# Kernel tuning notes

Measured on AMD Instinct MI355X. Metric: run time of the kernel, lower is better.

Reference implementation:

```python
import jax, jax.numpy as jnp
import numpy as np
from jax import lax

TAU = 0.1
DT = 0.001
UNITS = 1024
B, T = 16, 2048


def setup_inputs() -> dict:
    key = jax.random.key(0)
    inputs = jax.random.normal(key, (B, T, UNITS), dtype=jnp.float32)
    level_var = jnp.zeros((1, UNITS), dtype=jnp.float32)
    e = np.exp(-DT / TAU)
    smoothing_init = np.log(e / (1.0 - e)).astype(np.float32)
    smoothing_var = jnp.ones((1, UNITS), dtype=jnp.float32) * smoothing_init
    return {"inputs": inputs, "level_var": level_var, "smoothing_var": smoothing_var}


def reference(inputs, level_var, smoothing_var):
    # inputs: [B, T, U]; level_var, smoothing_var: [1, U]
    s = jax.nn.sigmoid(smoothing_var)  # [1, U]
    level0 = jnp.broadcast_to(level_var, (inputs.shape[0], inputs.shape[2]))  # [B, U]

    def step(level, x_t):
        new = (1.0 - s) * x_t + s * level  # [B, U]
        return new, new

    _, levels = lax.scan(step, level0, jnp.swapaxes(inputs, 0, 1))  # [T, B, U]
    return jnp.swapaxes(levels, 0, 1)  # [B, T, U]
```

## Files before the change

### kernel.cpp

```cpp
#include <hip/hip_runtime.h>


constexpr int B = 16;
constexpr int T = 2048;
constexpr int U = 1024;
constexpr int D = 32;

__global__ __launch_bounds__(64, 1) void lowpass_kernel(
    const float* __restrict__ in,
    const float* __restrict__ level0,
    const float* __restrict__ smooth,
    float* __restrict__ out)
{
    const int lane = threadIdx.x;
    const int blk  = blockIdx.x;
    const int b    = blk >> 4;
    const int ublk = blk & 15;
    const int u    = (ublk << 6) + lane;

    const float sm  = smooth[u];
    const float s   = 1.0f / (1.0f + expf(-sm));
    const float oms = 1.0f - s;
    float level     = level0[u];

    const size_t base = (size_t)b * T * U + u;
    const float* __restrict__ ip = in  + base;
    float*       __restrict__ op = out + base;

    float buf[D];
    #pragma unroll
    for (int i = 0; i < D; ++i) buf[i] = ip[(size_t)i * U];

    int t = 0;
    for (; t < T - D; t += D) {
        #pragma unroll
        for (int j = 0; j < D; ++j) {
            float x = buf[j];
            buf[j] = ip[(size_t)(t + D + j) * U];
            level = fmaf(s, level, oms * x);
            op[(size_t)(t + j) * U] = level;
        }
    }
    #pragma unroll
    for (int j = 0; j < D; ++j) {
        float x = buf[j];
        level = fmaf(s, level, oms * x);
        op[(size_t)(t + j) * U] = level;
    }
}

extern "C" void kernel_launch(void* const* d_in, const int* in_sizes, int n_in,
                              void* d_out, int out_size, void* d_ws, size_t ws_size,
                              hipStream_t stream) {
    const float* in     = (const float*)d_in[0];
    const float* level0 = (const float*)d_in[1];
    const float* smooth = (const float*)d_in[2];
    float* out          = (float*)d_out;

    dim3 grid(B * (U / 64));
    dim3 block(64);
    hipLaunchKernelGGL(lowpass_kernel, grid, block, 0, stream,
                       in, level0, smooth, out);
}
```

Measured before the change: 253.7 us.

## Split time axis into chunks with two-pass chunked linear-recurrence scan

Splits the sequential recurrence over T into 8 chunks. A first kernel computes each chunk's zero-initialized end state into workspace. A second kernel combines the prior chunk states using s^L to get each chunk's starting level, then rescans the chunk and writes outputs. This raises the number of independent wavefronts eightfold to hide the serial dependency latency, at the cost of reading the input twice and an extra launch.

```diff
diff --git a/kernel.cpp b/kernel.cpp
--- a/kernel.cpp
+++ b/kernel.cpp
@@ -1,51 +1,107 @@
 #include <hip/hip_runtime.h>
 
 
-constexpr int B = 16;
-constexpr int T = 2048;
-constexpr int U = 1024;
-constexpr int D = 32;
+constexpr int B  = 16;
+constexpr int T  = 2048;
+constexpr int U  = 1024;
+constexpr int C  = 8;
+constexpr int L  = T / C;
+constexpr int D1 = 32;
+constexpr int D2 = 16;
+constexpr int BU = B * U;
 
-__global__ __launch_bounds__(64, 1) void lowpass_kernel(
+__device__ __forceinline__ float sigmoidf(float x) {
+    return 1.0f / (1.0f + __expf(-x));
+}
+
+__global__ __launch_bounds__(64, 2) void lowpass_partial(
+    const float* __restrict__ in,
+    const float* __restrict__ smooth,
+    float* __restrict__ P)
+{
+    const int lane = threadIdx.x;
+    const int blk  = blockIdx.x;
+    const int c    = blk >> 8;
+    const int r    = blk & 255;
+    const int b    = r >> 4;
+    const int u    = ((r & 15) << 6) + lane;
+
+    const float s   = sigmoidf(smooth[u]);
+    const float oms = 1.0f - s;
+
+    const float* __restrict__ ip = in + (size_t)b * T * U + (size_t)(c * L) * U + u;
+
+    float lv = 0.0f;
+    float buf[D1];
+    #pragma unroll
+    for (int i = 0; i < D1; ++i) buf[i] = ip[(size_t)i * U];
+
+    int t = 0;
+    for (; t < L - D1; t += D1) {
+        #pragma unroll
+        for (int j = 0; j < D1; ++j) {
+            float x = buf[j];
+            buf[j] = ip[(size_t)(t + D1 + j) * U];
+            lv = fmaf(s, lv, oms * x);
+        }
+    }
+    #pragma unroll
+    for (int j = 0; j < D1; ++j) {
+        lv = fmaf(s, lv, oms * buf[j]);
+    }
+
+    P[(size_t)c * BU + (size_t)b * U + u] = lv;
+}
+
+__global__ __launch_bounds__(64, 2) void lowpass_scan(
     const float* __restrict__ in,
     const float* __restrict__ level0,
     const float* __restrict__ smooth,
+    const float* __restrict__ P,
     float* __restrict__ out)
 {
     const int lane = threadIdx.x;
     const int blk  = blockIdx.x;
-    const int b    = blk >> 4;
-    const int ublk = blk & 15;
-    const int u    = (ublk << 6) + lane;
+    const int c    = blk >> 8;
+    const int r    = blk & 255;
+    const int b    = r >> 4;
+    const int u    = ((r & 15) << 6) + lane;
+    const int chain = b * U + u;
 
-    const float sm  = smooth[u];
-    const float s   = 1.0f / (1.0f + expf(-sm));
+    const float s   = sigmoidf(smooth[u]);
     const float oms = 1.0f - s;
-    float level     = level0[u];
 
-    const size_t base = (size_t)b * T * U + u;
+    float sL = s;
+    #pragma unroll
+    for (int i = 0; i < 8; ++i) sL *= sL;
+
+    float lv = level0[u];
+    for (int i = 0; i < c; ++i) {
+        lv = fmaf(sL, lv, P[(size_t)i * BU + chain]);
+    }
+
+    const size_t base = (size_t)b * T * U + (size_t)(c * L) * U + u;
     const float* __restrict__ ip = in  + base;
     float*       __restrict__ op = out + base;
 
-    float buf[D];
+    float buf[D2];
     #pragma unroll
-    for (int i = 0; i < D; ++i) buf[i] = ip[(size_t)i * U];
+    for (int i = 0; i < D2; ++i) buf[i] = ip[(size_t)i * U];
 
     int t = 0;
-    for (; t < T - D; t += D) {
+    for (; t < L - D2; t += D2) {
         #pragma unroll
-        for (int j = 0; j < D; ++j) {
+        for (int j = 0; j < D2; ++j) {
             float x = buf[j];
-            buf[j] = ip[(size_t)(t + D + j) * U];
-            level = fmaf(s, level, oms * x);
-            op[(size_t)(t + j) * U] = level;
+            buf[j] = ip[(size_t)(t + D2 + j) * U];
+            lv = fmaf(s, lv, oms * x);
+            op[(size_t)(t + j) * U] = lv;
         }
     }
     #pragma unroll
-    for (int j = 0; j < D; ++j) {
-        float x = buf[j];
-        level = fmaf(s, level, oms * x);
-        op[(size_t)(t + j) * U] = level;
+    for (int j = 0; j < D2; ++j) {
+        lv = fmaf(s, lv, oms * buf[j]);
+        op[(size_t)(t + j) * U] = lv;
     }
 }
 
@@ -56,9 +112,11 @@
     const float* level0 = (const float*)d_in[1];
     const float* smooth = (const float*)d_in[2];
     float* out          = (float*)d_out;
+    float* P            = (float*)d_ws;
 
-    dim3 grid(B * (U / 64));
     dim3 block(64);
-    hipLaunchKernelGGL(lowpass_kernel, grid, block, 0, stream,
-                       in, level0, smooth, out);
+    dim3 grid(C * (BU / 64));
+
+    hipLaunchKernelGGL(lowpass_partial, grid, block, 0, stream, in, smooth, P);
+    hipLaunchKernelGGL(lowpass_scan,    grid, block, 0, stream, in, level0, smooth, P, out);
 }
```

Result: no change. 252.7 us (-0.4%).

## Split time scan into chunked two-pass parallel scan with float4 vectorization

Applied to the files above, without the earlier changes.

Replaces the sequential per-unit scan over all 2048 steps with a two-kernel chunked scan. The first kernel computes each 64-step chunk's zero-start partial state, and the second combines earlier chunk carries using s^64 before rescanning its chunk and writing outputs. Loads and stores are vectorized to float4. This exposes far more parallelism, since the old grid had only 256 single-wave blocks, at the cost of reading the input twice and an extra launch. It also uses a less accurate fast exp and a power-based carry combine.

```diff
diff --git a/kernel.cpp b/kernel.cpp
--- a/kernel.cpp
+++ b/kernel.cpp
@@ -1,64 +1,152 @@
 #include <hip/hip_runtime.h>
 
 
-constexpr int B = 16;
-constexpr int T = 2048;
-constexpr int U = 1024;
-constexpr int D = 32;
+constexpr int B  = 16;
+constexpr int T  = 2048;
+constexpr int U  = 1024;
+constexpr int C  = 32;
+constexpr int L  = T / C;
+constexpr int D  = 16;
+constexpr int U4 = U / 4;
+constexpr int G  = B * (U / 256);
+constexpr int P4N = B * U / 4;
 
-__global__ __launch_bounds__(64, 1) void lowpass_kernel(
-    const float* __restrict__ in,
-    const float* __restrict__ level0,
-    const float* __restrict__ smooth,
-    float* __restrict__ out)
+__device__ __forceinline__ float sigmoidf(float x) {
+    return 1.0f / (1.0f + __expf(-x));
+}
+
+__global__ __launch_bounds__(64, 2) void lowpass_partial(
+    const float4* __restrict__ in4,
+    const float4* __restrict__ smooth4,
+    float4* __restrict__ P4)
 {
     const int lane = threadIdx.x;
     const int blk  = blockIdx.x;
-    const int b    = blk >> 4;
-    const int ublk = blk & 15;
-    const int u    = (ublk << 6) + lane;
+    const int c    = blk >> 6;
+    const int g    = blk & 63;
+    const int b    = g >> 2;
+    const int ublk = g & 3;
+    const int u4   = ublk * 64 + lane;
 
-    const float sm  = smooth[u];
-    const float s   = 1.0f / (1.0f + expf(-sm));
-    const float oms = 1.0f - s;
-    float level     = level0[u];
+    const float4 smv = smooth4[u4];
+    const float sx = sigmoidf(smv.x), sy = sigmoidf(smv.y),
+                sz = sigmoidf(smv.z), sw = sigmoidf(smv.w);
+    const float ox = 1.0f - sx, oy = 1.0f - sy, oz = 1.0f - sz, ow = 1.0f - sw;
 
-    const size_t base = (size_t)b * T * U + u;
-    const float* __restrict__ ip = in  + base;
-    float*       __restrict__ op = out + base;
+    const float4* __restrict__ ip =
+        in4 + ((size_t)b * T + (size_t)c * L) * U4 + u4;
 
-    float buf[D];
+    float lx = 0.f, ly = 0.f, lz = 0.f, lw = 0.f;
+    float4 buf[D];
     #pragma unroll
-    for (int i = 0; i < D; ++i) buf[i] = ip[(size_t)i * U];
+    for (int i = 0; i < D; ++i) buf[i] = ip[(size_t)i * U4];
 
     int t = 0;
-    for (; t < T - D; t += D) {
+    for (; t < L - D; t += D) {
         #pragma unroll
         for (int j = 0; j < D; ++j) {
-            float x = buf[j];
-            buf[j] = ip[(size_t)(t + D + j) * U];
-            level = fmaf(s, level, oms * x);
-            op[(size_t)(t + j) * U] = level;
+            float4 x = buf[j];
+            buf[j] = ip[(size_t)(t + D + j) * U4];
+            lx = fmaf(sx, lx, ox * x.x);
+            ly = fmaf(sy, ly, oy * x.y);
+            lz = fmaf(sz, lz, oz * x.z);
+            lw = fmaf(sw, lw, ow * x.w);
         }
     }
     #pragma unroll
     for (int j = 0; j < D; ++j) {
-        float x = buf[j];
-        level = fmaf(s, level, oms * x);
-        op[(size_t)(t + j) * U] = level;
+        float4 x = buf[j];
+        lx = fmaf(sx, lx, ox * x.x);
+        ly = fmaf(sy, ly, oy * x.y);
+        lz = fmaf(sz, lz, oz * x.z);
+        lw = fmaf(sw, lw, ow * x.w);
+    }
+
+    P4[(size_t)c * P4N + (size_t)g * 64 + lane] = make_float4(lx, ly, lz, lw);
+}
+
+__global__ __launch_bounds__(64, 2) void lowpass_scan(
+    const float4* __restrict__ in4,
+    const float4* __restrict__ level04,
+    const float4* __restrict__ smooth4,
+    const float4* __restrict__ P4,
+    float4* __restrict__ out4)
+{
+    const int lane = threadIdx.x;
+    const int blk  = blockIdx.x;
+    const int c    = blk >> 6;
+    const int g    = blk & 63;
+    const int b    = g >> 2;
+    const int ublk = g & 3;
+    const int u4   = ublk * 64 + lane;
+
+    const float4 smv = smooth4[u4];
+    const float sx = sigmoidf(smv.x), sy = sigmoidf(smv.y),
+                sz = sigmoidf(smv.z), sw = sigmoidf(smv.w);
+    const float ox = 1.0f - sx, oy = 1.0f - sy, oz = 1.0f - sz, ow = 1.0f - sw;
+
+    float pLx = sx, pLy = sy, pLz = sz, pLw = sw;
+    #pragma unroll
+    for (int i = 0; i < 6; ++i) {
+        pLx *= pLx; pLy *= pLy; pLz *= pLz; pLw *= pLw;
+    }
+
+    float4 l0 = level04[u4];
+    float ex = l0.x, ey = l0.y, ez = l0.z, ew = l0.w;
+    for (int i = 0; i < c; ++i) {
+        float4 p = P4[(size_t)i * P4N + (size_t)g * 64 + lane];
+        ex = fmaf(pLx, ex, p.x);
+        ey = fmaf(pLy, ey, p.y);
+        ez = fmaf(pLz, ez, p.z);
+        ew = fmaf(pLw, ew, p.w);
+    }
+
+    const size_t base = ((size_t)b * T + (size_t)c * L) * U4 + u4;
+    const float4* __restrict__ ip = in4  + base;
+    float4*       __restrict__ op = out4 + base;
+
+    float4 buf[D];
+    #pragma unroll
+    for (int i = 0; i < D; ++i) buf[i] = ip[(size_t)i * U4];
+
+    int t = 0;
+    for (; t < L - D; t += D) {
+        #pragma unroll
+        for (int j = 0; j < D; ++j) {
+            float4 x = buf[j];
+            buf[j] = ip[(size_t)(t + D + j) * U4];
+            ex = fmaf(sx, ex, ox * x.x);
+            ey = fmaf(sy, ey, oy * x.y);
+            ez = fmaf(sz, ez, oz * x.z);
+            ew = fmaf(sw, ew, ow * x.w);
+            op[(size_t)(t + j) * U4] = make_float4(ex, ey, ez, ew);
+        }
+    }
+    #pragma unroll
+    for (int j = 0; j < D; ++j) {
+        float4 x = buf[j];
+        ex = fmaf(sx, ex, ox * x.x);
+        ey = fmaf(sy, ey, oy * x.y);
+        ez = fmaf(sz, ez, oz * x.z);
+        ew = fmaf(sw, ew, ow * x.w);
+        op[(size_t)(t + j) * U4] = make_float4(ex, ey, ez, ew);
     }
 }
 
 extern "C" void kernel_launch(void* const* d_in, const int* in_sizes, int n_in,
                               void* d_out, int out_size, void* d_ws, size_t ws_size,
                               hipStream_t stream) {
-    const float* in     = (const float*)d_in[0];
-    const float* level0 = (const float*)d_in[1];
-    const float* smooth = (const float*)d_in[2];
-    float* out          = (float*)d_out;
+    const float4* in4     = (const float4*)d_in[0];
+    const float4* level04 = (const float4*)d_in[1];
+    const float4* smooth4 = (const float4*)d_in[2];
+    float4* out4          = (float4*)d_out;
+    float4* P4            = (float4*)d_ws;
 
-    dim3 grid(B * (U / 64));
     dim3 block(64);
-    hipLaunchKernelGGL(lowpass_kernel, grid, block, 0, stream,
-                       in, level0, smooth, out);
+    dim3 grid(C * G);
+
+    hipLaunchKernelGGL(lowpass_partial, grid, block, 0, stream,
+                       in4, smooth4, P4);
+    hipLaunchKernelGGL(lowpass_scan, grid, block, 0, stream,
+                       in4, level04, smooth4, P4, out4);
 }
```

Result: slower. 262.7 us (+3.5%).
